# Kernel tuning notes

Measured on AMD Instinct MI355X. Metric: run time of the kernel, lower is better.

Reference implementation:

```python
import jax, jax.numpy as jnp
import numpy as np

NEAR = 0.0
SCENE_SCALE = 1.0
OPACITY_THRESHOLD = 0.01
EARLY_TERM = 1e-4
N_RAYS = 4096
N_SAMPLES = 256
GRID = 128
FEAT = 64
HID = 128
RGB_HID = 64


def mip360_contract(c):
    # Mip-NeRF 360 scene contraction; safe norm avoids NaN grads in the unused branch.
    norm = jnp.linalg.norm(c, axis=-1, keepdims=True)
    safe = jnp.maximum(norm, 1e-12)
    return jnp.where(norm <= 1.0, c, (2.0 - 1.0 / safe) * c / safe) / 2.0


def unbounded_stepping(near, uniform_range, n):
    ts = jnp.linspace(0.0, 1.0 - 1.0 / (n + 2), n + 1)
    ts = jnp.where(ts < 0.5, 2.0 * ts, 1.0 / (2.0 - 2.0 * ts)) * uniform_range + near
    return ts[:-1], ts[1:] - ts[:-1]


def grid_sample_3d(grid, coords):
    # torch F.grid_sample bilinear, align_corners=False, zeros padding.
    # grid [D,H,W]; coords [...,3] = (x,y,z) with x->W, y->H, z->D, in [-1,1].
    D, H, W = grid.shape
    x, y, z = coords[..., 0], coords[..., 1], coords[..., 2]
    ix = ((x + 1.0) * W - 1.0) * 0.5
    iy = ((y + 1.0) * H - 1.0) * 0.5
    iz = ((z + 1.0) * D - 1.0) * 0.5
    ix0, iy0, iz0 = jnp.floor(ix), jnp.floor(iy), jnp.floor(iz)
    fx, fy, fz = ix - ix0, iy - iy0, iz - iz0
    out = jnp.zeros(x.shape, grid.dtype)
    for dz in (0, 1):
        for dy in (0, 1):
            for dx in (0, 1):
                cx, cy, cz = ix0 + dx, iy0 + dy, iz0 + dz
                w = (fx if dx else 1.0 - fx) * (fy if dy else 1.0 - fy) * (fz if dz else 1.0 - fz)
                valid = (cx >= 0) & (cx < W) & (cy >= 0) & (cy < H) & (cz >= 0) & (cz < D)
                g = grid[jnp.clip(cz, 0, D - 1).astype(jnp.int32),
                         jnp.clip(cy, 0, H - 1).astype(jnp.int32),
                         jnp.clip(cx, 0, W - 1).astype(jnp.int32)]
                out = out + jnp.where(valid, w * g, 0.0)
    return out


def setup_inputs() -> dict:
    key = jax.random.key(0)
    ks = jax.random.split(key, 8)
    rays_o = jax.random.normal(ks[0], (N_RAYS, 3), jnp.float32) * 0.3
    rd = jax.random.normal(ks[1], (N_RAYS, 3), jnp.float32)
    rays_d = rd / jnp.linalg.norm(rd, axis=-1, keepdims=True)
    grid = jax.random.uniform(ks[2], (GRID, GRID, GRID), jnp.float32)
    lin = lambda k, fan_in, shape: jax.random.normal(k, shape, jnp.float32) / np.sqrt(fan_in).astype(np.float32)
    return dict(
        rays_o=rays_o, rays_d=rays_d, grid=grid,
        f_w1=lin(ks[3], 3, (3, HID)), f_b1=jnp.zeros((HID,), jnp.float32),
        f_w2=lin(ks[4], HID, (HID, FEAT)), f_b2=jnp.zeros((FEAT,), jnp.float32),
        s_w=lin(ks[5], FEAT, (FEAT, 1)), s_b=jnp.zeros((1,), jnp.float32),
        r_w1=lin(ks[6], FEAT + 3, (FEAT + 3, RGB_HID)), r_b1=jnp.zeros((RGB_HID,), jnp.float32),
        r_w2=lin(ks[7], RGB_HID, (RGB_HID, 3)), r_b2=jnp.zeros((3,), jnp.float32),
        n_samples=N_SAMPLES,
    )


def reference(rays_o, rays_d, grid, f_w1, f_b1, f_w2, f_b2, s_w, s_b, r_w1, r_b1, r_w2, r_b2, n_samples):
    n_rays = rays_o.shape[0]
    t, dist = unbounded_stepping(NEAR, SCENE_SCALE, n_samples)               # [S], [S]
    samples = rays_o[:, None, :] + rays_d[:, None, :] * t[None, :, None]     # [R,S,3]
    samples = mip360_contract(samples)
    occ = grid_sample_3d(grid, samples)                                      # [R,S]
    mask = occ > OPACITY_THRESHOLD
    # feature module (dense compute, masked write as in samples_features[mask] = ...)
    feat = jax.nn.relu(samples @ f_w1 + f_b1) @ f_w2 + f_b2                  # [R,S,F]
    feat = jnp.where(mask[..., None], feat, 0.0)
    sigma = jnp.where(mask, jax.nn.softplus(feat @ s_w + s_b)[..., 0], 0.0)  # [R,S]
    a = -sigma * dist[None, :]
    trans = jnp.concatenate(
        [jnp.ones((n_rays, 1), a.dtype), jnp.exp(jnp.cumsum(a, axis=1))[:, :-1]], axis=1)
    weights = trans * (1.0 - jnp.exp(a))                                     # [R,S]
    mask2 = mask & (trans > EARLY_TERM)
    dirs = jnp.broadcast_to(rays_d[:, None, :], samples.shape)
    h = jax.nn.relu(jnp.concatenate([feat, dirs], axis=-1) @ r_w1 + r_b1)
    rgb = jax.nn.sigmoid(h @ r_w2 + r_b2) * weights[..., None]
    rgb = jnp.where(mask2[..., None], rgb, 0.0)
    return rgb.sum(axis=1)                                                   # [R,3]
```

## Files before the change

kernel.cpp:

```cpp
#include <hip/hip_runtime.h>
#include <hip/hip_bf16.h>
#include <math.h>
#include <stdint.h>

#define S    256
#define GN   128

typedef __attribute__((ext_vector_type(8))) short  short8;
typedef __attribute__((ext_vector_type(4))) float  floatx4;
typedef __attribute__((ext_vector_type(2))) float  float2v;

#define WS_BHI 0
#define WS_RW1 16384
#define WS_B2S 24576
#define WS_WS2 24592
#define WS_W1P 25104
#define WS_W2E 27152

__device__ __forceinline__ unsigned short bf16_rtne(float f) {
    uint32_t u = __builtin_bit_cast(uint32_t, f);
    uint32_t r = (u + 0x7fffu + ((u >> 16) & 1u)) >> 16;
    return (unsigned short)r;
}
__device__ __forceinline__ uint32_t cvt_pk_bf16(float a, float b) {
    float2 hh; hh.x = a; hh.y = b;
    __hip_bfloat162 pk = __float22bfloat162_rn(hh);
    uint32_t u; __builtin_memcpy(&u, &pk, 4);
    return u;
}

__global__ __launch_bounds__(256)
void nerf_prep(const float* __restrict__ f_w1, const float* __restrict__ f_b1,
               const float* __restrict__ f_w2, const float* __restrict__ f_b2,
               const float* __restrict__ s_w,  const float* __restrict__ s_b,
               const float* __restrict__ r_w1, const float* __restrict__ r_w2,
               unsigned char* __restrict__ ws)
{
    const int tid = threadIdx.x;
    if (tid < 128) {
        float acc = 0.0f;
        for (int n = 0; n < 64; ++n) acc += f_w2[tid * 64 + n] * s_w[n];
        ((float*)(ws + WS_WS2))[tid] = acc;
    } else if (tid == 128) {
        float acc = s_b[0];
        for (int n = 0; n < 64; ++n) acc += f_b2[n] * s_w[n];
        *(float*)(ws + WS_B2S) = acc;
    }
    {
        float* w1pk = (float*)(ws + WS_W1P);
        for (int pp = tid; pp < 64; pp += 256) {
            int k0 = 2 * pp, k1 = 2 * pp + 1;
            w1pk[pp * 8 + 0] = f_w1[k0];       w1pk[pp * 8 + 1] = f_w1[k1];
            w1pk[pp * 8 + 2] = f_w1[128 + k0]; w1pk[pp * 8 + 3] = f_w1[128 + k1];
            w1pk[pp * 8 + 4] = f_w1[256 + k0]; w1pk[pp * 8 + 5] = f_w1[256 + k1];
            w1pk[pp * 8 + 6] = f_b1[k0];       w1pk[pp * 8 + 7] = f_b1[k1];
        }
    }

    unsigned short* bhi = (unsigned short*)(ws + WS_BHI);
    for (int i = tid; i < 8192; i += 256) {
        int j = i & 7, L = (i >> 3) & 63, g = i >> 9;
        int tn = g & 3, kc = g >> 2;
        int q = L >> 4, cc = L & 15;
        int k = kc * 32 + q * 8 + j;
        bhi[i] = bf16_rtne(f_w2[k * 64 + tn * 16 + cc]);
    }
    unsigned short* rw = (unsigned short*)(ws + WS_RW1);
    for (int i = tid; i < 4096; i += 256) {
        int j = i & 7, L = (i >> 3) & 63, g = i >> 9;
        int tn = g & 3, ks = g >> 2;
        int q = L >> 4, cc = L & 15;
        int k = ks * 32 + q * 8 + j;
        rw[i] = bf16_rtne(r_w1[k * 64 + tn * 16 + cc]);
    }
    unsigned short* w2e = (unsigned short*)(ws + WS_W2E);
    for (int i = tid; i < 1024; i += 256) {
        int j = i & 7, L = (i >> 3) & 63, kf = i >> 9;
        int q = L >> 4, ch = L & 15;
        int k = kf * 32 + q * 8 + j;
        w2e[i] = (ch < 3) ? bf16_rtne(r_w2[k * 3 + ch]) : (unsigned short)0;
    }
}

__global__ __launch_bounds__(256, 4)
void nerf_mfma(const float* __restrict__ rays_o,
               const float* __restrict__ rays_d,
               const float* __restrict__ grid,
               const float* __restrict__ f_b2,
               const float* __restrict__ r_w1,
               const float* __restrict__ r_b1,
               const float* __restrict__ r_b2,
               const unsigned char* __restrict__ ws,
               float* __restrict__ out)
{
    __shared__ __align__(16) unsigned short fh[256 * 64];
    unsigned char* fhB = (unsigned char*)fh;

    const int tid   = threadIdx.x;
    const int ray   = blockIdx.x;
    const int lane  = tid & 63;
    const int wv    = tid >> 6;
    const int q     = lane >> 4;
    const int c     = lane & 15;
    const int mbase = wv * 64;
    const int d01   = 72 - ((c >> 3) << 4);

    if (tid < 128) {
        ((float4*)(fhB + 4096))[tid] = ((const float4*)(ws + WS_W1P))[tid];
        ((float*)(fhB + 6144))[tid]  = ((const float*)(ws + WS_WS2))[tid];
    }

    const float stop = 1.0f - 1.0f / (float)(S + 2);
    const float step = stop / (float)S;
    float u0 = (float)tid * step;
    float u1 = (float)(tid + 1) * step;
    float t    = (u0 < 0.5f) ? 2.0f * u0 : 1.0f / (2.0f - 2.0f * u0);
    float tn_  = (u1 < 0.5f) ? 2.0f * u1 : 1.0f / (2.0f - 2.0f * u1);
    float dist = tn_ - t;

    float ox = rays_o[ray * 3 + 0], oy = rays_o[ray * 3 + 1], oz = rays_o[ray * 3 + 2];
    float dxv = rays_d[ray * 3 + 0], dyv = rays_d[ray * 3 + 1], dzv = rays_d[ray * 3 + 2];

    float px = ox + dxv * t, py = oy + dyv * t, pz = oz + dzv * t;
    float nrm = sqrtf(px * px + py * py + pz * pz);
    float scale = (nrm <= 1.0f) ? 0.5f : (2.0f - 1.0f / nrm) / nrm * 0.5f;
    float cx = px * scale, cy = py * scale, cz = pz * scale;

    float ix = ((cx + 1.0f) * (float)GN - 1.0f) * 0.5f;
    float iy = ((cy + 1.0f) * (float)GN - 1.0f) * 0.5f;
    float iz = ((cz + 1.0f) * (float)GN - 1.0f) * 0.5f;
    float fx0 = floorf(ix), fy0 = floorf(iy), fz0 = floorf(iz);
    float fx = ix - fx0, fy = iy - fy0, fz = iz - fz0;
    int x0 = (int)fx0, y0 = (int)fy0, z0 = (int)fz0;
    int x1 = x0 + 1, y1 = y0 + 1, z1 = z0 + 1;

    float wxv[2], wyv[2], wzv[2];
    wxv[0] = (x0 >= 0) ? (1.0f - fx) : 0.0f;  wxv[1] = (x1 < GN) ? fx : 0.0f;
    wyv[0] = (y0 >= 0) ? (1.0f - fy) : 0.0f;  wyv[1] = (y1 < GN) ? fy : 0.0f;
    wzv[0] = (z0 >= 0) ? (1.0f - fz) : 0.0f;  wzv[1] = (z1 < GN) ? fz : 0.0f;
    int xc[2], yb[2], zb[2];
    xc[0] = (x0 < 0) ? 0 : x0;              xc[1] = (x1 > GN - 1) ? GN - 1 : x1;
    yb[0] = ((y0 < 0) ? 0 : y0) * GN;       yb[1] = ((y1 > GN - 1) ? GN - 1 : y1) * GN;
    zb[0] = ((z0 < 0) ? 0 : z0) * (GN*GN);  zb[1] = ((z1 > GN - 1) ? GN - 1 : z1) * (GN*GN);

    float occ = 0.0f;
    #pragma unroll
    for (int dzc = 0; dzc < 2; ++dzc)
    #pragma unroll
    for (int dyc = 0; dyc < 2; ++dyc)
    #pragma unroll
    for (int dxc = 0; dxc < 2; ++dxc) {
        float w = (wxv[dxc] * wyv[dyc]) * wzv[dzc];
        occ += w * grid[zb[dzc] + yb[dyc] + xc[dxc]];
    }
    bool maskA = occ > 0.01f;

    __syncthreads();

    const unsigned short* __restrict__ bhiP = (const unsigned short*)(ws + WS_BHI);
    float sgv[4] = {0.0f, 0.0f, 0.0f, 0.0f};

    #pragma unroll 1
    for (int ph = 0; ph < 2; ++ph) {
        float cxs[2], cys[2], czs[2];
        #pragma unroll
        for (int tm = 0; tm < 2; ++tm) {
            int src = (ph * 2 + tm) * 16 + c;
            cxs[tm] = __shfl(cx, src, 64);
            cys[tm] = __shfl(cy, src, 64);
            czs[tm] = __shfl(cz, src, 64);
        }

        floatx4 acc[2][4];
        {
            float b2v[4];
            #pragma unroll
            for (int tn = 0; tn < 4; ++tn) b2v[tn] = f_b2[tn * 16 + c];
            #pragma unroll
            for (int tm = 0; tm < 2; ++tm)
                #pragma unroll
                for (int tn = 0; tn < 4; ++tn) {
                    floatx4 v; v[0] = b2v[tn]; v[1] = b2v[tn]; v[2] = b2v[tn]; v[3] = b2v[tn];
                    acc[tm][tn] = v;
                }
        }
        float2v sig2[2];
        sig2[0][0] = 0.0f; sig2[0][1] = 0.0f;
        sig2[1][0] = 0.0f; sig2[1][1] = 0.0f;

        #pragma unroll 2
        for (int kc = 0; kc < 4; ++kc) {
            const int k0  = kc * 32 + q * 8;
            const int pp0 = kc * 16 + q * 4;
            const float4* w1q4 = (const float4*)(fhB + 4096 + pp0 * 32);
            float ws2r[8];
            *(float4*)(ws2r)     = *(const float4*)(fhB + 6144 + k0 * 4);
            *(float4*)(ws2r + 4) = *(const float4*)(fhB + 6144 + k0 * 4 + 16);

            uint32_t packed[2][4];
            #pragma unroll
            for (int p = 0; p < 4; ++p) {
                float4 q0 = w1q4[2 * p];
                float4 q1 = w1q4[2 * p + 1];
                float2v wx2 = {q0.x, q0.y};
                float2v wy2 = {q0.z, q0.w};
                float2v wz2 = {q1.x, q1.y};
                float2v bb2 = {q1.z, q1.w};
                float2v wsp = {ws2r[2 * p], ws2r[2 * p + 1]};
                #pragma unroll
                for (int tm = 0; tm < 2; ++tm) {
                    float2v h2 = bb2;
                    h2 = __builtin_elementwise_fma((float2v){cxs[tm], cxs[tm]}, wx2, h2);
                    h2 = __builtin_elementwise_fma((float2v){cys[tm], cys[tm]}, wy2, h2);
                    h2 = __builtin_elementwise_fma((float2v){czs[tm], czs[tm]}, wz2, h2);
                    h2 = __builtin_elementwise_max(h2, (float2v){0.0f, 0.0f});
                    sig2[tm] = __builtin_elementwise_fma(h2, wsp, sig2[tm]);
                    packed[tm][p] = cvt_pk_bf16(h2[0], h2[1]);
                }
            }
            short8 Ah[2];
            #pragma unroll
            for (int tm = 0; tm < 2; ++tm) {
                uint4 v4 = {packed[tm][0], packed[tm][1], packed[tm][2], packed[tm][3]};
                Ah[tm] = __builtin_bit_cast(short8, v4);
            }
            const int bbase = (kc * 4) * 512 + lane * 8;
            #pragma unroll
            for (int tn = 0; tn < 4; ++tn) {
                short8 bh = *(const short8*)(bhiP + bbase + tn * 512);
                #pragma unroll
                for (int tm = 0; tm < 2; ++tm)
                    acc[tm][tn] = __builtin_amdgcn_mfma_f32_16x16x32_bf16(Ah[tm], bh, acc[tm][tn], 0, 0, 0);
            }
        }

        if (ph == 1) __syncthreads();

        #pragma unroll
        for (int tm = 0; tm < 2; ++tm)
            #pragma unroll
            for (int tn = 0; tn < 4; ++tn)
                #pragma unroll
                for (int pr = 0; pr < 2; ++pr) {
                    uint32_t u = cvt_pk_bf16(acc[tm][tn][2 * pr], acc[tm][tn][2 * pr + 1]);
                    int m0 = mbase + (ph * 2 + tm) * 16 + q * 4 + 2 * pr;
                    int i0 = m0 * 64 + c + (((tn * 2) ^ (m0 & 7)) << 3);
                    fh[i0]       = (unsigned short)u;
                    fh[i0 + d01] = (unsigned short)(u >> 16);
                }
        {
            float s0 = sig2[0][0] + sig2[0][1];
            s0 += __shfl_xor(s0, 16);
            s0 += __shfl_xor(s0, 32);
            float s1 = sig2[1][0] + sig2[1][1];
            s1 += __shfl_xor(s1, 16);
            s1 += __shfl_xor(s1, 32);
            if (ph == 0) { sgv[0] = s0; sgv[1] = s1; }
            else         { sgv[2] = s0; sgv[3] = s1; }
        }
    }

    float av;
    {
        float b2s = *(const float*)(ws + WS_B2S);
        float s01  = (q & 1) ? sgv[1] : sgv[0];
        float s23  = (q & 1) ? sgv[3] : sgv[2];
        float sa = ((q & 2) ? s23 : s01) + b2s;
        float sg = maskA ? (fmaxf(sa, 0.0f) + __logf(1.0f + __expf(-fabsf(sa)))) : 0.0f;
        av = -sg * dist;
    }

    float hd[4];
    #pragma unroll
    for (int tn = 0; tn < 4; ++tn) {
        int n = tn * 16 + c;
        hd[tn] = r_b1[n] + dxv * r_w1[64 * 64 + n] + dyv * r_w1[65 * 64 + n] + dzv * r_w1[66 * 64 + n];
    }

    float v = av;
    #pragma unroll
    for (int off = 1; off < 64; off <<= 1) {
        float u2 = __shfl_up(v, off);
        if (lane >= off) v += u2;
    }
    if (lane == 63 && wv < 3) out[ray * 3 + wv] = v;
    __syncthreads();
    float sw0 = out[ray * 3 + 0];
    float sw1 = out[ray * 3 + 1];
    float sw2 = out[ray * 3 + 2];
    float basev = ((wv > 0) ? sw0 : 0.0f) + ((wv > 1) ? sw1 : 0.0f)
                + ((wv > 2) ? sw2 : 0.0f);
    float excl = __shfl_up(v, 1);
    if (lane == 0) excl = 0.0f;
    float cum    = basev + excl;
    float trans  = __expf(cum);
    float weight = trans * (1.0f - __expf(av));
    bool  mask2  = maskA && (trans > 1e-4f);

    const unsigned short* __restrict__ rwP = (const unsigned short*)(ws + WS_RW1);

    #pragma unroll 1
    for (int ph = 0; ph < 2; ++ph) {
        short8 afr[2][2];
        #pragma unroll
        for (int tm = 0; tm < 2; ++tm)
            #pragma unroll
            for (int ks = 0; ks < 2; ++ks) {
                int m = mbase + (ph * 2 + tm) * 16 + c;
                int gl = ks * 4 + q;
                afr[tm][ks] = *(const short8*)&fh[m * 64 + ((gl ^ (m & 7)) << 3)];
            }

        floatx4 acc[2][4];
        #pragma unroll
        for (int tm = 0; tm < 2; ++tm)
            #pragma unroll
            for (int tn = 0; tn < 4; ++tn) {
                floatx4 z; z[0] = 0.0f; z[1] = 0.0f; z[2] = 0.0f; z[3] = 0.0f;
                acc[tm][tn] = z;
            }
        #pragma unroll
        for (int ks = 0; ks < 2; ++ks)
            #pragma unroll
            for (int tn = 0; tn < 4; ++tn) {
                short8 rb = *(const short8*)(rwP + ((ks * 4 + tn) * 64 + lane) * 8);
                #pragma unroll
                for (int tm = 0; tm < 2; ++tm)
                    acc[tm][tn] = __builtin_amdgcn_mfma_f32_16x16x32_bf16(afr[tm][ks], rb, acc[tm][tn], 0, 0, 0);
            }

        __builtin_amdgcn_wave_barrier();
        #pragma unroll
        for (int tm = 0; tm < 2; ++tm)
            #pragma unroll
            for (int tn = 0; tn < 4; ++tn)
                #pragma unroll
                for (int pr = 0; pr < 2; ++pr) {
                    float2v a2 = {acc[tm][tn][2 * pr], acc[tm][tn][2 * pr + 1]};
                    a2 = a2 + (float2v){hd[tn], hd[tn]};
                    a2 = __builtin_elementwise_max(a2, (float2v){0.0f, 0.0f});
                    uint32_t u = cvt_pk_bf16(a2[0], a2[1]);
                    int m0 = mbase + (ph * 2 + tm) * 16 + q * 4 + 2 * pr;
                    int i0 = m0 * 64 + c + (((tn * 2) ^ (m0 & 7)) << 3);
                    fh[i0]       = (unsigned short)u;
                    fh[i0 + d01] = (unsigned short)(u >> 16);
                }
    }
    __builtin_amdgcn_wave_barrier();

    float wm = mask2 ? weight : 0.0f;
    float wgt[4];
    #pragma unroll
    for (int tn = 0; tn < 4; ++tn) wgt[tn] = __shfl(wm, tn * 16 + c, 64);

    const unsigned short* __restrict__ w2eP = (const unsigned short*)(ws + WS_W2E);
    short8 w2f[2];
    w2f[0] = *(const short8*)(w2eP + (0 * 64 + lane) * 8);
    w2f[1] = *(const short8*)(w2eP + (1 * 64 + lane) * 8);

    floatx4 eacc[4];
    #pragma unroll
    for (int tn = 0; tn < 4; ++tn) {
        floatx4 z; z[0] = 0.0f; z[1] = 0.0f; z[2] = 0.0f; z[3] = 0.0f;
        eacc[tn] = z;
    }
    #pragma unroll
    for (int kf = 0; kf < 2; ++kf)
        #pragma unroll
        for (int tn = 0; tn < 4; ++tn) {
            int m = mbase + tn * 16 + c;
            int gl = kf * 4 + q;
            short8 hb = *(const short8*)&fh[m * 64 + ((gl ^ (m & 7)) << 3)];
            eacc[tn] = __builtin_amdgcn_mfma_f32_16x16x32_bf16(w2f[kf], hb, eacc[tn], 0, 0, 0);
        }

    float r = 0.0f, g = 0.0f, b = 0.0f;
    if (q == 0) {
        float rb0 = r_b2[0], rb1 = r_b2[1], rb2v = r_b2[2];
        #pragma unroll
        for (int tn = 0; tn < 4; ++tn) {
            float wgtv = wgt[tn];
            r += wgtv / (1.0f + __expf(-(eacc[tn][0] + rb0)));
            g += wgtv / (1.0f + __expf(-(eacc[tn][1] + rb1)));
            b += wgtv / (1.0f + __expf(-(eacc[tn][2] + rb2v)));
        }
    }
    #pragma unroll
    for (int off = 8; off > 0; off >>= 1) {
        r += __shfl_xor(r, off);
        g += __shfl_xor(g, off);
        b += __shfl_xor(b, off);
    }
    if (lane == 0) {
        float* pp = (float*)fhB + wv * 2048;
        pp[0] = r; pp[1] = g; pp[2] = b;
    }
    __syncthreads();
    if (tid == 0) {
        float* pf = (float*)fhB;
        out[ray * 3 + 0] = pf[0] + pf[2048] + pf[4096] + pf[6144];
        out[ray * 3 + 1] = pf[1] + pf[2049] + pf[4097] + pf[6145];
        out[ray * 3 + 2] = pf[2] + pf[2050] + pf[4098] + pf[6146];
    }
}

extern "C" void kernel_launch(void* const* d_in, const int* in_sizes, int n_in,
                              void* d_out, int out_size, void* d_ws, size_t ws_size,
                              hipStream_t stream) {
    const int n_rays = in_sizes[0] / 3;
    nerf_prep<<<1, 256, 0, stream>>>(
        (const float*)d_in[3], (const float*)d_in[4], (const float*)d_in[5],
        (const float*)d_in[6], (const float*)d_in[7], (const float*)d_in[8],
        (const float*)d_in[9], (const float*)d_in[11], (unsigned char*)d_ws);
    nerf_mfma<<<n_rays, 256, 0, stream>>>(
        (const float*)d_in[0],  (const float*)d_in[1],  (const float*)d_in[2],
        (const float*)d_in[6],  (const float*)d_in[9],  (const float*)d_in[10],
        (const float*)d_in[12],
        (const unsigned char*)d_ws, (float*)d_out);
}
```

Before: 172.2 us.

## Software-pipeline weight loads and move rgb layer-1 GEMM before the scan barrier

Fully unrolls the feature-MLP k-loop with double-buffered B-fragment global loads, so the next chunk's weights are fetched while the current chunk computes. Hoists the bias loads to the top of the kernel. Moves the rgb first-layer MFMA stage ahead of the __syncthreads that publishes per-wave scan totals, so that stage overlaps the barrier wait. This raises register pressure through the extra live B fragments and the hoisted rw1 fragment preloads.

```diff
diff --git a/kernel.cpp b/kernel.cpp
--- a/kernel.cpp
+++ b/kernel.cpp
@@ -110,6 +110,9 @@
         ((float*)(fhB + 6144))[tid]  = ((const float*)(ws + WS_WS2))[tid];
     }
 
+    float b2s  = *(const float*)(ws + WS_B2S);
+    float b2v0 = f_b2[c], b2v1 = f_b2[16 + c], b2v2 = f_b2[32 + c], b2v3 = f_b2[48 + c];
+
     const float stop = 1.0f - 1.0f / (float)(S + 2);
     const float step = stop / (float)S;
     float u0 = (float)tid * step;
@@ -160,6 +163,52 @@
     const unsigned short* __restrict__ bhiP = (const unsigned short*)(ws + WS_BHI);
     float sgv[4] = {0.0f, 0.0f, 0.0f, 0.0f};
 
+#define LOADB(D0, D1, D2, D3, KC) { \
+        const short8* bp_ = (const short8*)(bhiP + (KC) * 2048 + lane * 8); \
+        D0 = bp_[0]; D1 = bp_[64]; D2 = bp_[128]; D3 = bp_[192]; }
+
+#define KC_STEP(KC, B0, B1, B2, B3, ...) { \
+        const int k0_  = (KC) * 32 + q * 8; \
+        const int pp0_ = (KC) * 16 + q * 4; \
+        const float4* w1q4_ = (const float4*)(fhB + 4096 + pp0_ * 32); \
+        float ws2r_[8]; \
+        *(float4*)(ws2r_)     = *(const float4*)(fhB + 6144 + k0_ * 4); \
+        *(float4*)(ws2r_ + 4) = *(const float4*)(fhB + 6144 + k0_ * 4 + 16); \
+        __VA_ARGS__ \
+        uint32_t packed_[2][4]; \
+        _Pragma("unroll") \
+        for (int p = 0; p < 4; ++p) { \
+            float4 q0_ = w1q4_[2 * p]; \
+            float4 q1_ = w1q4_[2 * p + 1]; \
+            float2v wx2_ = {q0_.x, q0_.y}; \
+            float2v wy2_ = {q0_.z, q0_.w}; \
+            float2v wz2_ = {q1_.x, q1_.y}; \
+            float2v bb2_ = {q1_.z, q1_.w}; \
+            float2v wsp_ = {ws2r_[2 * p], ws2r_[2 * p + 1]}; \
+            _Pragma("unroll") \
+            for (int tm = 0; tm < 2; ++tm) { \
+                float2v h2_ = bb2_; \
+                h2_ = __builtin_elementwise_fma((float2v){cxs[tm], cxs[tm]}, wx2_, h2_); \
+                h2_ = __builtin_elementwise_fma((float2v){cys[tm], cys[tm]}, wy2_, h2_); \
+                h2_ = __builtin_elementwise_fma((float2v){czs[tm], czs[tm]}, wz2_, h2_); \
+                h2_ = __builtin_elementwise_max(h2_, (float2v){0.0f, 0.0f}); \
+                sig2[tm] = __builtin_elementwise_fma(h2_, wsp_, sig2[tm]); \
+                packed_[tm][p] = cvt_pk_bf16(h2_[0], h2_[1]); \
+            } \
+        } \
+        uint4 v40_ = {packed_[0][0], packed_[0][1], packed_[0][2], packed_[0][3]}; \
+        uint4 v41_ = {packed_[1][0], packed_[1][1], packed_[1][2], packed_[1][3]}; \
+        short8 Ah0_ = __builtin_bit_cast(short8, v40_); \
+        short8 Ah1_ = __builtin_bit_cast(short8, v41_); \
+        acc[0][0] = __builtin_amdgcn_mfma_f32_16x16x32_bf16(Ah0_, B0, acc[0][0], 0, 0, 0); \
+        acc[1][0] = __builtin_amdgcn_mfma_f32_16x16x32_bf16(Ah1_, B0, acc[1][0], 0, 0, 0); \
+        acc[0][1] = __builtin_amdgcn_mfma_f32_16x16x32_bf16(Ah0_, B1, acc[0][1], 0, 0, 0); \
+        acc[1][1] = __builtin_amdgcn_mfma_f32_16x16x32_bf16(Ah1_, B1, acc[1][1], 0, 0, 0); \
+        acc[0][2] = __builtin_amdgcn_mfma_f32_16x16x32_bf16(Ah0_, B2, acc[0][2], 0, 0, 0); \
+        acc[1][2] = __builtin_amdgcn_mfma_f32_16x16x32_bf16(Ah1_, B2, acc[1][2], 0, 0, 0); \
+        acc[0][3] = __builtin_amdgcn_mfma_f32_16x16x32_bf16(Ah0_, B3, acc[0][3], 0, 0, 0); \
+        acc[1][3] = __builtin_amdgcn_mfma_f32_16x16x32_bf16(Ah1_, B3, acc[1][3], 0, 0, 0); }
+
     #pragma unroll 1
     for (int ph = 0; ph < 2; ++ph) {
         float cxs[2], cys[2], czs[2];
@@ -172,67 +221,23 @@
         }
 
         floatx4 acc[2][4];
-        {
-            float b2v[4];
-            #pragma unroll
-            for (int tn = 0; tn < 4; ++tn) b2v[tn] = f_b2[tn * 16 + c];
-            #pragma unroll
-            for (int tm = 0; tm < 2; ++tm)
-                #pragma unroll
-                for (int tn = 0; tn < 4; ++tn) {
-                    floatx4 v; v[0] = b2v[tn]; v[1] = b2v[tn]; v[2] = b2v[tn]; v[3] = b2v[tn];
-                    acc[tm][tn] = v;
-                }
+        #pragma unroll
+        for (int tm = 0; tm < 2; ++tm) {
+            { floatx4 v_; v_[0]=b2v0; v_[1]=b2v0; v_[2]=b2v0; v_[3]=b2v0; acc[tm][0]=v_; }
+            { floatx4 v_; v_[0]=b2v1; v_[1]=b2v1; v_[2]=b2v1; v_[3]=b2v1; acc[tm][1]=v_; }
+            { floatx4 v_; v_[0]=b2v2; v_[1]=b2v2; v_[2]=b2v2; v_[3]=b2v2; acc[tm][2]=v_; }
+            { floatx4 v_; v_[0]=b2v3; v_[1]=b2v3; v_[2]=b2v3; v_[3]=b2v3; acc[tm][3]=v_; }
         }
         float2v sig2[2];
         sig2[0][0] = 0.0f; sig2[0][1] = 0.0f;
         sig2[1][0] = 0.0f; sig2[1][1] = 0.0f;
 
-        #pragma unroll 2
-        for (int kc = 0; kc < 4; ++kc) {
-            const int k0  = kc * 32 + q * 8;
-            const int pp0 = kc * 16 + q * 4;
-            const float4* w1q4 = (const float4*)(fhB + 4096 + pp0 * 32);
-            float ws2r[8];
-            *(float4*)(ws2r)     = *(const float4*)(fhB + 6144 + k0 * 4);
-            *(float4*)(ws2r + 4) = *(const float4*)(fhB + 6144 + k0 * 4 + 16);
-
-            uint32_t packed[2][4];
-            #pragma unroll
-            for (int p = 0; p < 4; ++p) {
-                float4 q0 = w1q4[2 * p];
-                float4 q1 = w1q4[2 * p + 1];
-                float2v wx2 = {q0.x, q0.y};
-                float2v wy2 = {q0.z, q0.w};
-                float2v wz2 = {q1.x, q1.y};
-                float2v bb2 = {q1.z, q1.w};
-                float2v wsp = {ws2r[2 * p], ws2r[2 * p + 1]};
-                #pragma unroll
-                for (int tm = 0; tm < 2; ++tm) {
-                    float2v h2 = bb2;
-                    h2 = __builtin_elementwise_fma((float2v){cxs[tm], cxs[tm]}, wx2, h2);
-                    h2 = __builtin_elementwise_fma((float2v){cys[tm], cys[tm]}, wy2, h2);
-                    h2 = __builtin_elementwise_fma((float2v){czs[tm], czs[tm]}, wz2, h2);
-                    h2 = __builtin_elementwise_max(h2, (float2v){0.0f, 0.0f});
-                    sig2[tm] = __builtin_elementwise_fma(h2, wsp, sig2[tm]);
-                    packed[tm][p] = cvt_pk_bf16(h2[0], h2[1]);
-                }
-            }
-            short8 Ah[2];
-            #pragma unroll
-            for (int tm = 0; tm < 2; ++tm) {
-                uint4 v4 = {packed[tm][0], packed[tm][1], packed[tm][2], packed[tm][3]};
-                Ah[tm] = __builtin_bit_cast(short8, v4);
-            }
-            const int bbase = (kc * 4) * 512 + lane * 8;
-            #pragma unroll
-            for (int tn = 0; tn < 4; ++tn) {
-                short8 bh = *(const short8*)(bhiP + bbase + tn * 512);
-                #pragma unroll
-                for (int tm = 0; tm < 2; ++tm)
-                    acc[tm][tn] = __builtin_amdgcn_mfma_f32_16x16x32_bf16(Ah[tm], bh, acc[tm][tn], 0, 0, 0);
-            }
-        }
+        short8 bA0, bA1, bA2, bA3, bB0, bB1, bB2, bB3;
+        LOADB(bA0, bA1, bA2, bA3, 0)
+        KC_STEP(0, bA0, bA1, bA2, bA3, LOADB(bB0, bB1, bB2, bB3, 1))
+        KC_STEP(1, bB0, bB1, bB2, bB3, LOADB(bA0, bA1, bA2, bA3, 2))
+        KC_STEP(2, bA0, bA1, bA2, bA3, LOADB(bB0, bB1, bB2, bB3, 3))
+        KC_STEP(3, bB0, bB1, bB2, bB3, )
 
         if (ph == 1) __syncthreads();
 
@@ -259,10 +264,11 @@
             else         { sgv[2] = s0; sgv[3] = s1; }
         }
     }
+#undef KC_STEP
+#undef LOADB
 
     float av;
     {
-        float b2s = *(const float*)(ws + WS_B2S);
         float s01  = (q & 1) ? sgv[1] : sgv[0];
         float s23  = (q & 1) ? sgv[3] : sgv[2];
         float sa = ((q & 2) ? s23 : s01) + b2s;
@@ -270,6 +276,14 @@
         av = -sg * dist;
     }
 
+    float v = av;
+    #pragma unroll
+    for (int off = 1; off < 64; off <<= 1) {
+        float u2 = __shfl_up(v, off);
+        if (lane >= off) v += u2;
+    }
+    if (lane == 63 && wv < 3) out[ray * 3 + wv] = v;
+
     float hd[4];
     #pragma unroll
     for (int tn = 0; tn < 4; ++tn) {
@@ -277,13 +291,61 @@
         hd[tn] = r_b1[n] + dxv * r_w1[64 * 64 + n] + dyv * r_w1[65 * 64 + n] + dzv * r_w1[66 * 64 + n];
     }
 
-    float v = av;
-    #pragma unroll
-    for (int off = 1; off < 64; off <<= 1) {
-        float u2 = __shfl_up(v, off);
-        if (lane >= off) v += u2;
-    }
-    if (lane == 63 && wv < 3) out[ray * 3 + wv] = v;
+    const short8* __restrict__ rw8 = (const short8*)(ws + WS_RW1);
+
+    #pragma unroll 1
+    for (int ph = 0; ph < 2; ++ph) {
+        short8 rb[2][4];
+        #pragma unroll
+        for (int ks = 0; ks < 2; ++ks)
+            #pragma unroll
+            for (int tn = 0; tn < 4; ++tn)
+                rb[ks][tn] = rw8[(ks * 4 + tn) * 64 + lane];
+
+        short8 afr[2][2];
+        #pragma unroll
+        for (int tm = 0; tm < 2; ++tm)
+            #pragma unroll
+            for (int ks = 0; ks < 2; ++ks) {
+                int m = mbase + (ph * 2 + tm) * 16 + c;
+                int gl = ks * 4 + q;
+                afr[tm][ks] = *(const short8*)&fh[m * 64 + ((gl ^ (m & 7)) << 3)];
+            }
+
+        floatx4 acc[2][4];
+        #pragma unroll
+        for (int tm = 0; tm < 2; ++tm)
+            #pragma unroll
+            for (int tn = 0; tn < 4; ++tn) {
+                floatx4 z; z[0] = 0.0f; z[1] = 0.0f; z[2] = 0.0f; z[3] = 0.0f;
+                acc[tm][tn] = z;
+            }
+        #pragma unroll
+        for (int ks = 0; ks < 2; ++ks)
+            #pragma unroll
+            for (int tn = 0; tn < 4; ++tn)
+                #pragma unroll
+                for (int tm = 0; tm < 2; ++tm)
+                    acc[tm][tn] = __builtin_amdgcn_mfma_f32_16x16x32_bf16(afr[tm][ks], rb[ks][tn], acc[tm][tn], 0, 0, 0);
+
+        __builtin_amdgcn_wave_barrier();
+        #pragma unroll
+        for (int tm = 0; tm < 2; ++tm)
+            #pragma unroll
+            for (int tn = 0; tn < 4; ++tn)
+                #pragma unroll
+                for (int pr = 0; pr < 2; ++pr) {
+                    float2v a2 = {acc[tm][tn][2 * pr], acc[tm][tn][2 * pr + 1]};
+                    a2 = a2 + (float2v){hd[tn], hd[tn]};
+                    a2 = __builtin_elementwise_max(a2, (float2v){0.0f, 0.0f});
+                    uint32_t u = cvt_pk_bf16(a2[0], a2[1]);
+                    int m0 = mbase + (ph * 2 + tm) * 16 + q * 4 + 2 * pr;
+                    int i0 = m0 * 64 + c + (((tn * 2) ^ (m0 & 7)) << 3);
+                    fh[i0]       = (unsigned short)u;
+                    fh[i0 + d01] = (unsigned short)(u >> 16);
+                }
+    }
+
     __syncthreads();
     float sw0 = out[ray * 3 + 0];
     float sw1 = out[ray * 3 + 1];
@@ -296,57 +358,6 @@
     float trans  = __expf(cum);
     float weight = trans * (1.0f - __expf(av));
     bool  mask2  = maskA && (trans > 1e-4f);
-
-    const unsigned short* __restrict__ rwP = (const unsigned short*)(ws + WS_RW1);
-
-    #pragma unroll 1
-    for (int ph = 0; ph < 2; ++ph) {
-        short8 afr[2][2];
-        #pragma unroll
-        for (int tm = 0; tm < 2; ++tm)
-            #pragma unroll
-            for (int ks = 0; ks < 2; ++ks) {
-                int m = mbase + (ph * 2 + tm) * 16 + c;
-                int gl = ks * 4 + q;
-                afr[tm][ks] = *(const short8*)&fh[m * 64 + ((gl ^ (m & 7)) << 3)];
-            }
-
-        floatx4 acc[2][4];
-        #pragma unroll
-        for (int tm = 0; tm < 2; ++tm)
-            #pragma unroll
-            for (int tn = 0; tn < 4; ++tn) {
-                floatx4 z; z[0] = 0.0f; z[1] = 0.0f; z[2] = 0.0f; z[3] = 0.0f;
-                acc[tm][tn] = z;
-            }
-        #pragma unroll
-        for (int ks = 0; ks < 2; ++ks)
-            #pragma unroll
-            for (int tn = 0; tn < 4; ++tn) {
-                short8 rb = *(const short8*)(rwP + ((ks * 4 + tn) * 64 + lane) * 8);
-                #pragma unroll
-                for (int tm = 0; tm < 2; ++tm)
-                    acc[tm][tn] = __builtin_amdgcn_mfma_f32_16x16x32_bf16(afr[tm][ks], rb, acc[tm][tn], 0, 0, 0);
-            }
-
-        __builtin_amdgcn_wave_barrier();
-        #pragma unroll
-        for (int tm = 0; tm < 2; ++tm)
-            #pragma unroll
-            for (int tn = 0; tn < 4; ++tn)
-                #pragma unroll
-                for (int pr = 0; pr < 2; ++pr) {
-                    float2v a2 = {acc[tm][tn][2 * pr], acc[tm][tn][2 * pr + 1]};
-                    a2 = a2 + (float2v){hd[tn], hd[tn]};
-                    a2 = __builtin_elementwise_max(a2, (float2v){0.0f, 0.0f});
-                    uint32_t u = cvt_pk_bf16(a2[0], a2[1]);
-                    int m0 = mbase + (ph * 2 + tm) * 16 + q * 4 + 2 * pr;
-                    int i0 = m0 * 64 + c + (((tn * 2) ^ (m0 & 7)) << 3);
-                    fh[i0]       = (unsigned short)u;
-                    fh[i0 + d01] = (unsigned short)(u >> 16);
-                }
-    }
-    __builtin_amdgcn_wave_barrier();
 
     float wm = mask2 ? weight : 0.0f;
     float wgt[4];
```

Result: slower. 362.8 us (+110.6%).
